# Optimization experiments

Hardware: AMD Instinct MI355X
Metric: run time of the kernel (lower is better)

## Reference

```python
import jax, jax.numpy as jnp
import numpy as np

N, D, YD, L = 500000, 256, 50, 1000


def setup_inputs() -> dict:
    key = jax.random.key(0)
    k_x, k_l, k_y, k_w1, k_w2 = jax.random.split(key, 5)
    lim1 = 1.0 / np.sqrt(D)
    return {
        "x": jax.random.normal(k_x, (N, D), dtype=jnp.float32),
        "labels": jax.random.randint(k_l, (N,), 0, L, dtype=jnp.int32),
        "y": jax.random.uniform(k_y, (N, YD), dtype=jnp.float32),
        "w1": jax.random.uniform(k_w1, (D, 1), jnp.float32, -lim1, lim1),
        "b1": jnp.zeros((1,), jnp.float32),
        "w2": jax.random.uniform(k_w2, (D, YD), jnp.float32, -lim1, lim1),
        "b2": jnp.zeros((YD,), jnp.float32),
        "num_labels": L,
    }


def reference(x, labels, y, w1, b1, w2, b2, num_labels):
    # sigmoid-gated features: a = sigmoid(x @ w1 + b1) * x   [N, D]
    a = jax.nn.sigmoid(x @ w1 + b1) * x
    # segment counts per label (labels assumed dense 0..L-1, all present)
    counts = jax.ops.segment_sum(jnp.ones((x.shape[0],), x.dtype), labels,
                                 num_segments=num_labels)
    denom = jnp.maximum(counts, 1.0)[:, None]  # guard empty segments
    # segment mean of gated features  [L, D]
    res = jax.ops.segment_sum(a, labels, num_segments=num_labels) / denom
    # softmax(linear2(res))  [L, YD]
    prediction = jax.nn.softmax(res @ w2 + b2, axis=1)
    # segment mean of soft targets  [L, YD]
    y_mean = jax.ops.segment_sum(y, labels, num_segments=num_labels) / denom
    # torch CrossEntropyLoss with probability targets applies log_softmax
    # to its input (here: already-softmaxed prediction) -- faithful double softmax
    logp = jax.nn.log_softmax(prediction, axis=1)
    return -jnp.mean(jnp.sum(y_mean * logp, axis=1))
```

## Files before the change

### kernel.cpp

```cpp
#include <hip/hip_runtime.h>
#include <math.h>

#define NROWS 500000
#define DIM 256
#define YDIM 50
#define NLAB 1000

#define XT 64
#define NTX ((NROWS + XT - 1) / XT)
#define XBLOCKS 256
#define ASTRIDE 264
#define ZC 51

#define YT 128
#define NTY ((NROWS + YT - 1) / YT)
#define YBLOCKS 256

typedef __attribute__((ext_vector_type(8))) short frag_ab;
typedef __attribute__((ext_vector_type(4))) float frag_cd;

__device__ __forceinline__ float b2f(unsigned short u) {
    return __uint_as_float(((unsigned)u) << 16);
}
__device__ __forceinline__ unsigned short f2b(float f) {
    unsigned u = __float_as_uint(f);
    return (unsigned short)((u + 0x7fffu + ((u >> 16) & 1u)) >> 16);
}
__device__ __forceinline__ void bar_lds() {
    asm volatile("s_waitcnt lgkmcnt(0)\n\ts_barrier" ::: "memory");
}

__global__ __launch_bounds__(1024) void k_xstream(
    const float* __restrict__ x, const int* __restrict__ labels,
    const float* __restrict__ w1, const float* __restrict__ b1,
    const float* __restrict__ w2, unsigned short* __restrict__ zpart,
    float* __restrict__ out)
{
    __shared__ unsigned short sA[XT * ASTRIDE];
    __shared__ float zst[XT][52];
    __shared__ unsigned short accz[NLAB * YDIM];
    __shared__ int slab[2][XT];

    const int tid = threadIdx.x, lane = tid & 63, wib = tid >> 6;
    const int bid = blockIdx.x;
    const int mh = wib >> 2, jt = wib & 3;

    if (bid == 0 && tid == 0) out[0] = 0.0f;
    for (int k = tid; k < NLAB * YDIM / 2; k += 1024)
        reinterpret_cast<unsigned*>(accz)[k] = 0u;

    frag_ab bfr[8];
    {
        const int n = 16 * jt + (lane & 15);
        #pragma unroll
        for (int s = 0; s < 8; ++s) {
            const int k0 = 32 * s + (lane >> 4) * 8;
            #pragma unroll
            for (int i = 0; i < 8; ++i) {
                const int kk = k0 + i;
                float v = 0.f;
                if (n < YDIM)       v = w2[kk * YDIM + n];
                else if (n == YDIM) v = w1[kk];
                bfr[s][i] = (short)f2b(v);
            }
        }
    }
    const float b1v = b1[0];
    __syncthreads();

    auto PREF = [&](int t, float4* r) {
        #pragma unroll
        for (int k = 0; k < 4; ++k) {
            const int rg = t * XT + 4 * wib + k;
            r[k] = (rg < NROWS)
                 ? reinterpret_cast<const float4*>(x)[(size_t)rg * 64 + lane]
                 : make_float4(0.f, 0.f, 0.f, 0.f);
        }
    };
    auto LLAB = [&](int t) -> int {
        const int rg = t * XT + tid;
        return (tid < XT && rg < NROWS) ? labels[rg] : 0;
    };

    auto process = [&](int t, int pft, float4* r, int& lb, int par) {
        if (tid < XT) slab[par][tid] = lb;
        uint2 pk[4];
        #pragma unroll
        for (int k = 0; k < 4; ++k) {
            pk[k].x = (unsigned)f2b(r[k].x) | ((unsigned)f2b(r[k].y) << 16);
            pk[k].y = (unsigned)f2b(r[k].z) | ((unsigned)f2b(r[k].w) << 16);
        }
        PREF(pft, r);
        lb = LLAB(pft);
        const int row = 4 * wib;
        #pragma unroll
        for (int k = 0; k < 4; ++k)
            *reinterpret_cast<uint2*>(&sA[(row + k) * ASTRIDE + lane * 4]) = pk[k];
        bar_lds();

        frag_cd c = {0.f, 0.f, 0.f, 0.f};
        #pragma unroll
        for (int s = 0; s < 8; ++s) {
            frag_ab a = *reinterpret_cast<const frag_ab*>(
                &sA[(16 * mh + (lane & 15)) * ASTRIDE + 32 * s + (lane >> 4) * 8]);
            c = __builtin_amdgcn_mfma_f32_16x16x32_bf16(a, bfr[s], c, 0, 0, 0);
        }
        const int zr = 16 * mh + (lane >> 4) * 4;
        const int zc = 16 * jt + (lane & 15);
        if (zc < ZC) {
            zst[zr + 0][zc] = c[0]; zst[zr + 1][zc] = c[1];
            zst[zr + 2][zc] = c[2]; zst[zr + 3][zc] = c[3];
        }
        bar_lds();

        {
            const int lbl_lane = slab[par][lane];
            unsigned long long mask = __ballot((lbl_lane & 15) == wib);
            while (mask) {
                const int r2 = __builtin_ctzll(mask);
                mask &= mask - 1;
                const int lbv = __shfl(lbl_lane, r2);
                const float d = zst[r2][YDIM];
                const float g = 1.0f / (1.0f + __expf(-(d + b1v)));
                if (lane < YDIM) {
                    const int a = lbv * YDIM + lane;
                    accz[a] = f2b(b2f(accz[a]) + g * zst[r2][lane]);
                }
            }
        }
    };

    float4 rA[4], rB[4];
    PREF(bid, rA);
    PREF(bid + XBLOCKS, rB);
    int lbA = LLAB(bid), lbB = LLAB(bid + XBLOCKS);
    int par = 0;
    for (int t = bid; t < NTX; t += 2 * XBLOCKS) {
        process(t, t + 2 * XBLOCKS, rA, lbA, par); par ^= 1;
        if (t + XBLOCKS < NTX) {
            process(t + XBLOCKS, t + 3 * XBLOCKS, rB, lbB, par); par ^= 1;
        }
    }
    __syncthreads();
    unsigned short* zp = zpart + (size_t)bid * (NLAB * YDIM);
    for (int k = tid; k < NLAB * YDIM; k += 1024) zp[k] = accz[k];
}

__global__ __launch_bounds__(1024) void k_ystream(
    const float* __restrict__ y, const int* __restrict__ labels,
    unsigned short* __restrict__ ypart, int* __restrict__ gcnt)
{
    __shared__ unsigned short accy[NLAB * YDIM];
    __shared__ float yst[2][YT * YDIM];
    __shared__ int slab[2][YT];
    __shared__ int cnt[NLAB];

    const int tid = threadIdx.x, lane = tid & 63, wib = tid >> 6;
    const int bid = blockIdx.x;

    for (int k = tid; k < NLAB * YDIM / 2; k += 1024)
        reinterpret_cast<unsigned*>(accy)[k] = 0u;
    for (int k = tid; k < NLAB; k += 1024) cnt[k] = 0;
    __syncthreads();

    auto PREFY = [&](int t, float* v, int& myl) {
        const size_t base = (size_t)t * YT * YDIM;
        const int n = (t < NTY) ? (min(YT, NROWS - t * YT) * YDIM) : 0;
        #pragma unroll
        for (int i = 0; i < 7; ++i) {
            const int k = tid + i * 1024;
            v[i] = (k < n) ? y[base + k] : 0.f;
        }
        const int rg = t * YT + tid;
        myl = (tid < YT && t < NTY && rg < NROWS) ? labels[rg] : -1;
    };

    auto process = [&](int t, int pft, float* v, int& myl, int par) {
        #pragma unroll
        for (int i = 0; i < 7; ++i) {
            const int k = tid + i * 1024;
            if (k < YT * YDIM) yst[par][k] = v[i];
        }
        if (tid < YT) {
            const bool valid = (myl >= 0);
            slab[par][tid] = valid ? myl : 0;
            if (valid) atomicAdd(&cnt[myl], 1);
        }
        PREFY(pft, v, myl);
        bar_lds();

        {
            const int l0 = slab[par][lane];
            const int l1 = slab[par][64 + lane];
            unsigned long long m0 = __ballot((l0 & 15) == wib);
            unsigned long long m1 = __ballot((l1 & 15) == wib);
            while (m0) {
                const int r = __builtin_ctzll(m0); m0 &= m0 - 1;
                const int lb = __shfl(l0, r);
                if (lane < YDIM) {
                    const int a = lb * YDIM + lane;
                    accy[a] = f2b(b2f(accy[a]) + yst[par][r * YDIM + lane]);
                }
            }
            while (m1) {
                const int r = __builtin_ctzll(m1); m1 &= m1 - 1;
                const int lb = __shfl(l1, r);
                if (lane < YDIM) {
                    const int a = lb * YDIM + lane;
                    accy[a] = f2b(b2f(accy[a]) + yst[par][(64 + r) * YDIM + lane]);
                }
            }
        }
    };

    float vA[7], vB[7];
    int mA, mB;
    PREFY(bid, vA, mA);
    PREFY(bid + YBLOCKS, vB, mB);
    int par = 0;
    for (int t = bid; t < NTY; t += 2 * YBLOCKS) {
        process(t, t + 2 * YBLOCKS, vA, mA, par); par ^= 1;
        if (t + YBLOCKS < NTY) {
            process(t + YBLOCKS, t + 3 * YBLOCKS, vB, mB, par); par ^= 1;
        }
    }
    __syncthreads();
    unsigned short* yp = ypart + (size_t)bid * (NLAB * YDIM);
    for (int k = tid; k < NLAB * YDIM; k += 1024) yp[k] = accy[k];
    for (int k = tid; k < NLAB; k += 1024)
        if (cnt[k]) atomicAdd(&gcnt[k], cnt[k]);
}

__global__ __launch_bounds__(256) void k_finalize(
    const unsigned short* __restrict__ zpart,
    const unsigned short* __restrict__ ypart,
    const int* __restrict__ gcnt,
    const float* __restrict__ b2, float* __restrict__ out)
{
    const int tid = threadIdx.x, lane = tid & 63, grp = tid >> 6;
    const int k0 = blockIdx.x * 200;

    float zs = 0.f, ys = 0.f;
    if (tid < 200) {
        const size_t idx = (size_t)k0 + tid;
        #pragma unroll 4
        for (int p = 0; p < XBLOCKS; ++p) {
            zs += b2f(zpart[(size_t)p * (NLAB * YDIM) + idx]);
            ys += b2f(ypart[(size_t)p * (NLAB * YDIM) + idx]);
        }
    }
    __shared__ float zl[200], yl[200];
    if (tid < 200) { zl[tid] = zs; yl[tid] = ys; }
    __syncthreads();

    const int l = blockIdx.x * 4 + grp;
    const bool act = lane < YDIM;
    const float zv = act ? zl[grp * 50 + lane] : 0.f;
    const float yv = act ? yl[grp * 50 + lane] : 0.f;

    const float denom = fmaxf((float)gcnt[l], 1.0f);
    const float NEG = -3.402823466e38f;
    float logit = act ? (zv / denom + b2[lane]) : NEG;
    const float ymean = act ? (yv / denom) : 0.f;

    float m = logit;
    #pragma unroll
    for (int o = 32; o > 0; o >>= 1) m = fmaxf(m, __shfl_xor(m, o));
    float e = act ? __expf(logit - m) : 0.f;
    float s = e;
    #pragma unroll
    for (int o = 32; o > 0; o >>= 1) s += __shfl_xor(s, o);
    const float p = e / s;

    float pm = act ? p : NEG;
    float m2 = pm;
    #pragma unroll
    for (int o = 32; o > 0; o >>= 1) m2 = fmaxf(m2, __shfl_xor(m2, o));
    float e2 = act ? __expf(p - m2) : 0.f;
    float s2 = e2;
    #pragma unroll
    for (int o = 32; o > 0; o >>= 1) s2 += __shfl_xor(s2, o);
    const float logp = p - m2 - __logf(s2);

    float contrib = act ? ymean * logp : 0.f;
    #pragma unroll
    for (int o = 32; o > 0; o >>= 1) contrib += __shfl_xor(contrib, o);
    if (lane == 0) atomicAdd(out, -contrib / (float)NLAB);
}

extern "C" void kernel_launch(void* const* d_in, const int* in_sizes, int n_in,
                              void* d_out, int out_size, void* d_ws, size_t ws_size,
                              hipStream_t stream) {
    const float* x      = (const float*)d_in[0];
    const int*   labels = (const int*)  d_in[1];
    const float* y      = (const float*)d_in[2];
    const float* w1     = (const float*)d_in[3];
    const float* b1     = (const float*)d_in[4];
    const float* w2     = (const float*)d_in[5];
    const float* b2     = (const float*)d_in[6];
    float* out = (float*)d_out;

    int* gcnt = (int*)d_ws;
    unsigned short* zpart = (unsigned short*)((char*)d_ws + 4096);
    unsigned short* ypart = (unsigned short*)((char*)d_ws + 4096 +
                             (size_t)XBLOCKS * NLAB * YDIM * 2);

    hipMemsetAsync(gcnt, 0, NLAB * sizeof(int), stream);
    k_xstream<<<XBLOCKS, 1024, 0, stream>>>(x, labels, w1, b1, w2, zpart, out);
    k_ystream<<<YBLOCKS, 1024, 0, stream>>>(y, labels, ypart, gcnt);
    k_finalize<<<250, 256, 0, stream>>>(zpart, ypart, gcnt, b2, out);
}
```

Before: 195.9 us.

## Defer x-stream scatter by one tile and pack bf16 accumulator updates in pairs

In the x-stream kernel the per-label scatter of gated z rows now runs one tile late, reading from a double-buffered zst. This removes one LDS barrier per tile and lets the scatter overlap the next tile's staging and MFMA work. Both the x and y scatter loops now update two bf16 accumulators per lane with a single 32-bit LDS read-modify-write over 25 lanes instead of 50, which halves the LDS accesses per row. The cost is extra LDS for the second zst buffer and more complex barrier ordering, where correctness depends on the deferred scatter staying clear of buffer reuse.

```diff
diff --git a/kernel.cpp b/kernel.cpp
--- a/kernel.cpp
+++ b/kernel.cpp
@@ -36,9 +36,9 @@
     const float* __restrict__ w2, unsigned short* __restrict__ zpart,
     float* __restrict__ out)
 {
-    __shared__ unsigned short sA[XT * ASTRIDE];
-    __shared__ float zst[XT][52];
-    __shared__ unsigned short accz[NLAB * YDIM];
+    __shared__ __align__(16) unsigned short sA[XT * ASTRIDE];
+    __shared__ __align__(16) float zst[2][XT][52];
+    __shared__ __align__(16) unsigned short accz[NLAB * YDIM];
     __shared__ int slab[2][XT];
 
     const int tid = threadIdx.x, lane = tid & 63, wib = tid >> 6;
@@ -82,7 +82,31 @@
         return (tid < XT && rg < NROWS) ? labels[rg] : 0;
     };
 
-    auto process = [&](int t, int pft, float4* r, int& lb, int par) {
+    auto SCATTER = [&](int pp) {
+        const int lbl_lane = slab[pp][lane];
+        unsigned long long mask = __ballot((lbl_lane & 15) == wib);
+        while (mask) {
+            const int r2 = __builtin_ctzll(mask);
+            mask &= mask - 1;
+            const int lbv = __shfl(lbl_lane, r2);
+            const float d = zst[pp][r2][YDIM];
+            const float g = 1.0f / (1.0f + __expf(-(d + b1v)));
+            if (lane < 25) {
+                const float2 zv =
+                    *reinterpret_cast<const float2*>(&zst[pp][r2][2 * lane]);
+                unsigned* ap =
+                    reinterpret_cast<unsigned*>(&accz[lbv * YDIM + 2 * lane]);
+                const unsigned old = *ap;
+                const float lo = b2f((unsigned short)(old & 0xffffu)) + g * zv.x;
+                const float hi = b2f((unsigned short)(old >> 16))     + g * zv.y;
+                *ap = (unsigned)f2b(lo) | ((unsigned)f2b(hi) << 16);
+            }
+        }
+    };
+
+    int prevpar = -1;
+
+    auto process = [&](int pft, float4* r, int& lb, int par) {
         if (tid < XT) slab[par][tid] = lb;
         uint2 pk[4];
         #pragma unroll
@@ -108,26 +132,12 @@
         const int zr = 16 * mh + (lane >> 4) * 4;
         const int zc = 16 * jt + (lane & 15);
         if (zc < ZC) {
-            zst[zr + 0][zc] = c[0]; zst[zr + 1][zc] = c[1];
-            zst[zr + 2][zc] = c[2]; zst[zr + 3][zc] = c[3];
-        }
+            zst[par][zr + 0][zc] = c[0]; zst[par][zr + 1][zc] = c[1];
+            zst[par][zr + 2][zc] = c[2]; zst[par][zr + 3][zc] = c[3];
+        }
+        if (prevpar >= 0) SCATTER(prevpar);
+        prevpar = par;
         bar_lds();
-
-        {
-            const int lbl_lane = slab[par][lane];
-            unsigned long long mask = __ballot((lbl_lane & 15) == wib);
-            while (mask) {
-                const int r2 = __builtin_ctzll(mask);
-                mask &= mask - 1;
-                const int lbv = __shfl(lbl_lane, r2);
-                const float d = zst[r2][YDIM];
-                const float g = 1.0f / (1.0f + __expf(-(d + b1v)));
-                if (lane < YDIM) {
-                    const int a = lbv * YDIM + lane;
-                    accz[a] = f2b(b2f(accz[a]) + g * zst[r2][lane]);
-                }
-            }
-        }
     };
 
     float4 rA[4], rB[4];
@@ -136,11 +146,12 @@
     int lbA = LLAB(bid), lbB = LLAB(bid + XBLOCKS);
     int par = 0;
     for (int t = bid; t < NTX; t += 2 * XBLOCKS) {
-        process(t, t + 2 * XBLOCKS, rA, lbA, par); par ^= 1;
+        process(t + 2 * XBLOCKS, rA, lbA, par); par ^= 1;
         if (t + XBLOCKS < NTX) {
-            process(t + XBLOCKS, t + 3 * XBLOCKS, rB, lbB, par); par ^= 1;
+            process(t + 3 * XBLOCKS, rB, lbB, par); par ^= 1;
         }
     }
+    if (prevpar >= 0) SCATTER(prevpar);
     __syncthreads();
     unsigned short* zp = zpart + (size_t)bid * (NLAB * YDIM);
     for (int k = tid; k < NLAB * YDIM; k += 1024) zp[k] = accz[k];
@@ -150,8 +161,8 @@
     const float* __restrict__ y, const int* __restrict__ labels,
     unsigned short* __restrict__ ypart, int* __restrict__ gcnt)
 {
-    __shared__ unsigned short accy[NLAB * YDIM];
-    __shared__ float yst[2][YT * YDIM];
+    __shared__ __align__(16) unsigned short accy[NLAB * YDIM];
+    __shared__ __align__(16) float yst[2][YT * YDIM];
     __shared__ int slab[2][YT];
     __shared__ int cnt[NLAB];
 
@@ -175,7 +186,7 @@
         myl = (tid < YT && t < NTY && rg < NROWS) ? labels[rg] : -1;
     };
 
-    auto process = [&](int t, int pft, float* v, int& myl, int par) {
+    auto process = [&](int pft, float* v, int& myl, int par) {
         #pragma unroll
         for (int i = 0; i < 7; ++i) {
             const int k = tid + i * 1024;
@@ -197,17 +208,29 @@
             while (m0) {
                 const int r = __builtin_ctzll(m0); m0 &= m0 - 1;
                 const int lb = __shfl(l0, r);
-                if (lane < YDIM) {
-                    const int a = lb * YDIM + lane;
-                    accy[a] = f2b(b2f(accy[a]) + yst[par][r * YDIM + lane]);
+                if (lane < 25) {
+                    const float2 yv = *reinterpret_cast<const float2*>(
+                        &yst[par][r * YDIM + 2 * lane]);
+                    unsigned* ap =
+                        reinterpret_cast<unsigned*>(&accy[lb * YDIM + 2 * lane]);
+                    const unsigned old = *ap;
+                    const float lo = b2f((unsigned short)(old & 0xffffu)) + yv.x;
+                    const float hi = b2f((unsigned short)(old >> 16))     + yv.y;
+                    *ap = (unsigned)f2b(lo) | ((unsigned)f2b(hi) << 16);
                 }
             }
             while (m1) {
                 const int r = __builtin_ctzll(m1); m1 &= m1 - 1;
                 const int lb = __shfl(l1, r);
-                if (lane < YDIM) {
-                    const int a = lb * YDIM + lane;
-                    accy[a] = f2b(b2f(accy[a]) + yst[par][(64 + r) * YDIM + lane]);
+                if (lane < 25) {
+                    const float2 yv = *reinterpret_cast<const float2*>(
+                        &yst[par][(64 + r) * YDIM + 2 * lane]);
+                    unsigned* ap =
+                        reinterpret_cast<unsigned*>(&accy[lb * YDIM + 2 * lane]);
+                    const unsigned old = *ap;
+                    const float lo = b2f((unsigned short)(old & 0xffffu)) + yv.x;
+                    const float hi = b2f((unsigned short)(old >> 16))     + yv.y;
+                    *ap = (unsigned)f2b(lo) | ((unsigned)f2b(hi) << 16);
                 }
             }
         }
@@ -219,9 +242,9 @@
     PREFY(bid + YBLOCKS, vB, mB);
     int par = 0;
     for (int t = bid; t < NTY; t += 2 * YBLOCKS) {
-        process(t, t + 2 * YBLOCKS, vA, mA, par); par ^= 1;
+        process(t + 2 * YBLOCKS, vA, mA, par); par ^= 1;
         if (t + YBLOCKS < NTY) {
-            process(t + YBLOCKS, t + 3 * YBLOCKS, vB, mB, par); par ^= 1;
+            process(t + 3 * YBLOCKS, vB, mB, par); par ^= 1;
         }
     }
     __syncthreads();
```

Result: slower. 212.3 us (+8.4%).
